# Kernel tuning notes

Hardware: AMD Instinct MI355X
Metric: run time of the kernel (lower is better)

Reference implementation:

```python
import jax, jax.numpy as jnp
import numpy as np

D_MODEL = 1024
NUM_HEADS = 16
D_K = D_MODEL // NUM_HEADS
THETA = 10000.0


def apply_rope(x, positions):
    # x: [b, h, s, d_k]; positions: [b, s] int32
    half = D_K // 2
    inv_freq = THETA ** (-jnp.arange(half, dtype=jnp.float32) * 2.0 / D_K)  # [half]
    angles = positions[:, None, :, None].astype(jnp.float32) * inv_freq  # [b,1,s,half]
    cos, sin = jnp.cos(angles), jnp.sin(angles)
    x1 = x[..., 0::2]  # even dims
    x2 = x[..., 1::2]  # odd dims
    out_even = x1 * cos - x2 * sin
    out_odd = x1 * sin + x2 * cos
    # re-interleave
    out = jnp.stack([out_even, out_odd], axis=-1)
    return out.reshape(x.shape)


def setup_inputs() -> dict:
    key = jax.random.key(0)
    ks = jax.random.split(key, 5)
    b, s = 2, 2048
    scale = 0.02
    return {
        "x": jax.random.normal(ks[0], (b, s, D_MODEL), dtype=jnp.float32),
        "Wq": jax.random.normal(ks[1], (D_MODEL, D_MODEL), dtype=jnp.float32) * scale,
        "Wk": jax.random.normal(ks[2], (D_MODEL, D_MODEL), dtype=jnp.float32) * scale,
        "Wv": jax.random.normal(ks[3], (D_MODEL, D_MODEL), dtype=jnp.float32) * scale,
        "Wo": jax.random.normal(ks[4], (D_MODEL, D_MODEL), dtype=jnp.float32) * scale,
    }


def reference(x, Wq, Wk, Wv, Wo):
    b, s, _ = x.shape
    # Linear(d, d) applied as x @ W^T (torch Linear convention, no bias)
    Q = x @ Wq.T
    K = x @ Wk.T
    V = x @ Wv.T
    # split heads: [b, s, h*d] -> [b, h, s, d]
    split = lambda t: t.reshape(b, s, NUM_HEADS, D_K).transpose(0, 2, 1, 3)
    Q, K, V = split(Q), split(K), split(V)
    positions = jnp.broadcast_to(jnp.arange(s, dtype=jnp.int32), (b, s))
    Q = apply_rope(Q, positions)
    K = apply_rope(K, positions)
    scores = jnp.einsum('bhqd,bhkd->bhqk', Q, K) / jnp.sqrt(jnp.float32(D_K))
    causal = jnp.tril(jnp.ones((s, s), dtype=bool))
    scores = jnp.where(causal[None, None], scores, -jnp.inf)
    attn = jax.nn.softmax(scores, axis=-1)
    out = jnp.einsum('bhqk,bhkd->bhqd', attn, V)
    out = out.transpose(0, 2, 1, 3).reshape(b, s, D_MODEL)
    return out @ Wo.T
```

## Files before the change

### kernel.cpp

```cpp
#include <hip/hip_runtime.h>

typedef __attribute__((ext_vector_type(8))) short bf16x8;
typedef __attribute__((ext_vector_type(4))) float f32x4;
typedef __attribute__((ext_vector_type(16))) float f32x16;

typedef const __attribute__((address_space(1))) unsigned int gu32;
typedef __attribute__((address_space(3))) unsigned int lu32;

__device__ __forceinline__ void async16(const void* g, void* l) {
  __builtin_amdgcn_global_load_lds((gu32*)g, (lu32*)l, 16, 0, 0);
}

__device__ __forceinline__ unsigned short f2bf(float f) {
  unsigned int u = __float_as_uint(f);
  u += 0x7fffu + ((u >> 16) & 1u);
  return (unsigned short)(u >> 16);
}
__device__ __forceinline__ float b2f(unsigned short s) {
  return __uint_as_float(((unsigned int)s) << 16);
}
__device__ __forceinline__ unsigned int cvtpk(float lo, float hi) {
  unsigned int w;
  asm("v_cvt_pk_bf16_f32 %0, %1, %2" : "=v"(w) : "v"(lo), "v"(hi));
  return w;
}
__device__ __forceinline__ void plswap(unsigned int& x, unsigned int& y) {
  asm("v_permlane32_swap_b32 %0, %1" : "+v"(x), "+v"(y));
}
__device__ __forceinline__ float max3f(float a, float b, float c) {
  float d;
  asm("v_max3_f32 %0, %1, %2, %3" : "=v"(d) : "v"(a), "v"(b), "v"(c));
  return d;
}

__global__ __launch_bounds__(256) void cvt_k(const float* __restrict__ in,
                                             unsigned short* __restrict__ out,
                                             int n4) {
  int i = blockIdx.x * 256 + threadIdx.x;
  if (i >= n4) return;
  float4 v = ((const float4*)in)[i];
  ushort4 o;
  o.x = f2bf(v.x); o.y = f2bf(v.y); o.z = f2bf(v.z); o.w = f2bf(v.w);
  ((ushort4*)out)[i] = o;
}

__global__ __launch_bounds__(256) void cvtw_k(const float* __restrict__ Wq,
                                              const float* __restrict__ Wk,
                                              const float* __restrict__ Wv,
                                              const float* __restrict__ Wo,
                                              unsigned short* __restrict__ Wb,
                                              unsigned short* __restrict__ Wob) {
  int i = blockIdx.x * 256 + threadIdx.x;
  int wsel = i >> 18;
  int j = i & 0x3FFFF;
  const float* src = (wsel == 0) ? Wq : (wsel == 1) ? Wk : (wsel == 2) ? Wv : Wo;
  unsigned short* dst = (wsel == 0) ? Wb : (wsel == 1) ? Wb + (1 << 20)
                       : (wsel == 2) ? Wb + (2 << 20) : Wob;
  float4 v = ((const float4*)src)[j];
  ushort4 o;
  o.x = f2bf(v.x); o.y = f2bf(v.y); o.z = f2bf(v.z); o.w = f2bf(v.w);
  ((ushort4*)dst)[j] = o;
}

template <int WRITE_F32>
__global__ __launch_bounds__(256) void gemm_bt(const unsigned short* __restrict__ A,
                                               const unsigned short* __restrict__ B,
                                               void* __restrict__ Cp, int N, int K) {
  __shared__ __align__(16) unsigned short Al[3][128 * 32];
  __shared__ __align__(16) unsigned short Bl[3][128 * 32];
  const int t = threadIdx.x;
  const int w = t >> 6, l = t & 63;
  const int wm = w >> 1, wn = w & 1;
  const int lr = l & 15, lg = l >> 4;
  const long bm = (long)blockIdx.x * 128, bn = (long)blockIdx.y * 128;
  const int srow = t >> 2;
  const int c8 = t & 3;
  const int KT = K >> 5;
  f32x4 acc[4][4] = {};

  auto STAGE = [&](int ts) {
    const int bi = ts % 3;
    const int k0 = ts * 32;
    #pragma unroll
    for (int r = 0; r < 2; ++r) {
      int row = r * 64 + srow;
      async16(&A[(bm + row) * (long)K + k0 + c8 * 8], &Al[bi][row * 32 + c8 * 8]);
      async16(&B[(bn + row) * (long)K + k0 + c8 * 8], &Bl[bi][row * 32 + c8 * 8]);
    }
  };

  STAGE(0);
  STAGE(1);
  for (int kt = 0; kt < KT; ++kt) {
    const int cur = kt % 3;
    if (kt < KT - 1) asm volatile("s_waitcnt vmcnt(4)" ::: "memory");
    else             asm volatile("s_waitcnt vmcnt(0)" ::: "memory");
    __builtin_amdgcn_s_barrier();
    __builtin_amdgcn_sched_barrier(0);
    if (kt + 2 < KT) STAGE(kt + 2);
    bf16x8 af[4], bf[4];
    #pragma unroll
    for (int i = 0; i < 4; ++i) {
      af[i] = *(const bf16x8*)&Al[cur][(wm * 64 + i * 16 + lr) * 32 + lg * 8];
      bf[i] = *(const bf16x8*)&Bl[cur][(wn * 64 + i * 16 + lr) * 32 + lg * 8];
    }
    #pragma unroll
    for (int i = 0; i < 4; ++i)
      #pragma unroll
      for (int j = 0; j < 4; ++j)
        acc[i][j] = __builtin_amdgcn_mfma_f32_16x16x32_bf16(af[i], bf[j], acc[i][j], 0, 0, 0);
  }
  #pragma unroll
  for (int i = 0; i < 4; ++i)
    #pragma unroll
    for (int j = 0; j < 4; ++j)
      #pragma unroll
      for (int r = 0; r < 4; ++r) {
        long row = bm + wm * 64 + i * 16 + lg * 4 + r;
        long col = bn + wn * 64 + j * 16 + lr;
        float v = acc[i][j][r];
        if (WRITE_F32) ((float*)Cp)[row * N + col] = v;
        else ((unsigned short*)Cp)[row * N + col] = f2bf(v);
      }
}

__global__ __launch_bounds__(256) void rope_k(unsigned short* __restrict__ QKV) {
  __shared__ float csl[32], snl[32];
  const int row = blockIdx.x;
  const int s = row & 2047;
  const int t = threadIdx.x;
  if (t < 32) {
    float invf = exp2f((float)t * (-13.287712379549449f / 32.0f));
    float sn, cs;
    sincosf((float)s * invf, &sn, &cs);
    csl[t] = cs; snl[t] = sn;
  }
  __syncthreads();
  const int col0 = (t < 128) ? t * 8 : 1024 + (t - 128) * 8;
  const int i0 = (t & 7) * 4;
  unsigned short* p = &QKV[(size_t)row * 3072 + col0];
  bf16x8 v = *(const bf16x8*)p;
  bf16x8 o;
  #pragma unroll
  for (int j = 0; j < 4; ++j) {
    float x1 = b2f((unsigned short)v[2 * j]);
    float x2 = b2f((unsigned short)v[2 * j + 1]);
    float cs = csl[i0 + j], sn = snl[i0 + j];
    o[2 * j]     = (short)f2bf(x1 * cs - x2 * sn);
    o[2 * j + 1] = (short)f2bf(x1 * sn + x2 * cs);
  }
  *(bf16x8*)p = o;
}

__global__ __launch_bounds__(256) void vtr_k(const unsigned short* __restrict__ QKV,
                                             unsigned short* __restrict__ Vt) {
  __shared__ unsigned short tl[64][66];
  const int kt = blockIdx.x;
  const int bh = blockIdx.y;
  const int b = bh >> 4, h = bh & 15;
  const int t = threadIdx.x;
  const int row = t >> 3, c8 = t & 7;
  #pragma unroll
  for (int r = 0; r < 2; ++r) {
    int k = r * 32 + row;
    bf16x8 v = *(const bf16x8*)&QKV[((long)b * 2048 + kt * 64 + k) * 3072 + 2048 + h * 64 + c8 * 8];
    #pragma unroll
    for (int j = 0; j < 8; ++j) tl[c8 * 8 + j][k] = (unsigned short)v[j];
  }
  __syncthreads();
  #pragma unroll
  for (int r = 0; r < 2; ++r) {
    int d = r * 32 + row;
    ushort4 a, bq;
    a.x = tl[d][c8 * 8 + 0]; a.y = tl[d][c8 * 8 + 1];
    a.z = tl[d][c8 * 8 + 2]; a.w = tl[d][c8 * 8 + 3];
    bq.x = tl[d][c8 * 8 + 4]; bq.y = tl[d][c8 * 8 + 5];
    bq.z = tl[d][c8 * 8 + 6]; bq.w = tl[d][c8 * 8 + 7];
    long off = ((long)bh * 64 + d) * 2048 + kt * 64 + c8 * 8;
    *(ushort4*)&Vt[off] = a;
    *(ushort4*)&Vt[off + 4] = bq;
  }
}

__global__ __launch_bounds__(256) void attn_k(const unsigned short* __restrict__ QKV,
                                              const unsigned short* __restrict__ VtG,
                                              unsigned short* __restrict__ O) {
  __shared__ __align__(16) unsigned short Kl[3][64 * 64];
  __shared__ __align__(16) unsigned short Vl[3][64 * 64];
  const int t = threadIdx.x;
  const int w = t >> 6, l = t & 63;
  const int q31 = l & 31, hi = l >> 5;
  const int bh = blockIdx.x;
  const int y = (int)blockIdx.y;
  const int qt = (y < 8) ? (15 - y) : (y - 8);
  const int b = bh >> 4, h = bh & 15;
  const int Qb = qt * 128;
  const long rowb = (long)b * 2048;
  const int L = 3072;
  const int NT = 2 * qt + 2;
  const float cexp = 0.125f * 1.4426950408889634f;

  const int qmy = Qb + 32 * w + q31;
  const long qgrow = rowb + qmy;
  const int ktmax = (Qb + 32 * w) >> 6;

  bf16x8 qf[4];
  #pragma unroll
  for (int dk = 0; dk < 4; ++dk)
    qf[dk] = *(const bf16x8*)&QKV[qgrow * L + h * 64 + dk * 16 + hi * 8];

  bf16x8 onesf;
  #pragma unroll
  for (int j = 0; j < 8; ++j) onesf[j] = (short)0x3F80;

  float m_ = -1e30f;
  f32x16 oa[2], la;
  #pragma unroll
  for (int r = 0; r < 16; ++r) { oa[0][r] = 0.0f; oa[1][r] = 0.0f; la[r] = 0.0f; }

  auto STAGE = [&](int ts) {
    const int bi = ts % 3;
    const long kb = rowb + (long)ts * 64;
    const long vrowb = (long)bh * 64;
    #pragma unroll
    for (int r = 0; r < 2; ++r) {
      int row = w * 16 + r * 8 + (l >> 3);
      int c8s = ((l & 7) ^ (row & 7)) * 8;
      async16(&QKV[(kb + row) * L + 1024 + h * 64 + c8s], &Kl[bi][row * 64 + (l & 7) * 8]);
      async16(&VtG[(vrowb + row) * 2048 + ts * 64 + c8s], &Vl[bi][row * 64 + (l & 7) * 8]);
    }
  };

  auto QK = [&](f32x16 (&st)[2], int bi) {
    #pragma unroll
    for (int kt2 = 0; kt2 < 2; ++kt2)
      #pragma unroll
      for (int r = 0; r < 16; ++r) st[kt2][r] = 0.0f;
    __builtin_amdgcn_s_setprio(1);
    #pragma unroll
    for (int dk = 0; dk < 4; ++dk)
      #pragma unroll
      for (int kt2 = 0; kt2 < 2; ++kt2) {
        int krow = kt2 * 32 + q31;
        bf16x8 kfr = *(const bf16x8*)&Kl[bi][krow * 64 + (((2 * dk + hi) ^ (krow & 7)) * 8)];
        st[kt2] = __builtin_amdgcn_mfma_f32_32x32x16_bf16(kfr, qf[dk], st[kt2], 0, 0, 0);
      }
    __builtin_amdgcn_s_setprio(0);
  };

  auto SMPV = [&](f32x16 (&st)[2], int kt) {
    if (kt == ktmax) {
      #pragma unroll
      for (int kt2 = 0; kt2 < 2; ++kt2)
        #pragma unroll
        for (int r = 0; r < 16; ++r) {
          int kg = kt * 64 + kt2 * 32 + (r & 3) + 8 * (r >> 2) + 4 * hi;
          if (kg > qmy) st[kt2][r] = -1e30f;
        }
    }
    float m0[8];
    #pragma unroll
    for (int i = 0; i < 8; ++i)
      m0[i] = max3f(st[0][i], st[0][i + 8], fmaxf(st[1][i], st[1][i + 8]));
    float mt = max3f(max3f(m0[0], m0[1], m0[2]), max3f(m0[3], m0[4], m0[5]),
                     fmaxf(m0[6], m0[7]));
    if (__any((mt - m_) * cexp > 8.0f)) {
      float mg = fmaxf(mt, __shfl_xor(mt, 32, 64));
      float mn = fmaxf(m_, mg);
      float al = __builtin_amdgcn_exp2f((m_ - mn) * cexp);
      m_ = mn;
      la[0] *= al;
      #pragma unroll
      for (int dt = 0; dt < 2; ++dt)
        #pragma unroll
        for (int r = 0; r < 16; ++r) oa[dt][r] *= al;
    }
    const float mc = m_ * cexp;
    #pragma unroll
    for (int kt2 = 0; kt2 < 2; ++kt2)
      #pragma unroll
      for (int r = 0; r < 16; ++r)
        st[kt2][r] = __builtin_amdgcn_exp2f(fmaf(st[kt2][r], cexp, -mc));
    bf16x8 pfr[4];
    #pragma unroll
    for (int ks = 0; ks < 4; ++ks) {
      int tt = ks >> 1, gX = 2 * (ks & 1), gY = gX + 1;
      unsigned int x1 = cvtpk(st[tt][4 * gX + 0], st[tt][4 * gX + 1]);
      unsigned int y1 = cvtpk(st[tt][4 * gY + 0], st[tt][4 * gY + 1]);
      plswap(x1, y1);
      unsigned int x2 = cvtpk(st[tt][4 * gX + 2], st[tt][4 * gX + 3]);
      unsigned int y2 = cvtpk(st[tt][4 * gY + 2], st[tt][4 * gY + 3]);
      plswap(x2, y2);
      union { unsigned int u[4]; bf16x8 b; } cc;
      cc.u[0] = x1; cc.u[1] = x2; cc.u[2] = y1; cc.u[3] = y2;
      pfr[ks] = cc.b;
    }
    const int vb = kt % 3;
    __builtin_amdgcn_s_setprio(1);
    #pragma unroll
    for (int ks = 0; ks < 4; ++ks) {
      la = __builtin_amdgcn_mfma_f32_32x32x16_bf16(onesf, pfr[ks], la, 0, 0, 0);
      #pragma unroll
      for (int dt = 0; dt < 2; ++dt) {
        int vrow = dt * 32 + q31;
        bf16x8 vf = *(const bf16x8*)&Vl[vb][vrow * 64 + (((2 * ks + hi) ^ (vrow & 7)) * 8)];
        oa[dt] = __builtin_amdgcn_mfma_f32_32x32x16_bf16(vf, pfr[ks], oa[dt], 0, 0, 0);
      }
    }
    __builtin_amdgcn_s_setprio(0);
  };

  f32x16 stA[2], stB[2];

  STAGE(0);
  STAGE(1);
  asm volatile("s_waitcnt vmcnt(4)" ::: "memory");
  __builtin_amdgcn_s_barrier();
  __builtin_amdgcn_sched_barrier(0);
  QK(stA, 0);

  auto STEP = [&](f32x16 (&cur)[2], f32x16 (&nxt)[2], int kt) {
    asm volatile("s_waitcnt vmcnt(0)" ::: "memory");
    __builtin_amdgcn_s_barrier();
    __builtin_amdgcn_sched_barrier(0);
    if (kt + 1 < NT && kt + 1 <= ktmax) QK(nxt, (kt + 1) % 3);
    if (kt + 2 < NT) STAGE(kt + 2);
    if (kt <= ktmax) SMPV(cur, kt);
  };

  int kt = 0;
  while (kt < NT) {
    STEP(stA, stB, kt); ++kt;
    if (kt < NT) { STEP(stB, stA, kt); ++kt; }
  }

  float inv = 1.0f / la[0];
  #pragma unroll
  for (int dt = 0; dt < 2; ++dt)
    #pragma unroll
    for (int g = 0; g < 4; ++g) {
      ushort4 o4;
      o4.x = f2bf(oa[dt][4 * g + 0] * inv);
      o4.y = f2bf(oa[dt][4 * g + 1] * inv);
      o4.z = f2bf(oa[dt][4 * g + 2] * inv);
      o4.w = f2bf(oa[dt][4 * g + 3] * inv);
      *(ushort4*)&O[qgrow * 1024 + h * 64 + dt * 32 + 8 * g + 4 * hi] = o4;
    }
}

extern "C" void kernel_launch(void* const* d_in, const int* in_sizes, int n_in,
                              void* d_out, int out_size, void* d_ws, size_t ws_size,
                              hipStream_t stream) {
  const float* x  = (const float*)d_in[0];
  const float* Wq = (const float*)d_in[1];
  const float* Wk = (const float*)d_in[2];
  const float* Wv = (const float*)d_in[3];
  const float* Wo = (const float*)d_in[4];
  char* ws = (char*)d_ws;
  unsigned short* xb   = (unsigned short*)(ws);
  unsigned short* Wb   = (unsigned short*)(ws + (8u << 20));
  unsigned short* Wob  = (unsigned short*)(ws + (14u << 20));
  unsigned short* QKVb = (unsigned short*)(ws + (16u << 20));
  unsigned short* Ob   = (unsigned short*)(ws + (40u << 20));
  unsigned short* Vtg  = xb;

  cvt_k<<<4096, 256, 0, stream>>>(x, xb, 4096 * 1024 / 4);
  cvtw_k<<<4096, 256, 0, stream>>>(Wq, Wk, Wv, Wo, Wb, Wob);

  gemm_bt<0><<<dim3(32, 24), 256, 0, stream>>>(xb, Wb, QKVb, 3072, 1024);
  rope_k<<<4096, 256, 0, stream>>>(QKVb);
  vtr_k<<<dim3(32, 32), 256, 0, stream>>>(QKVb, Vtg);
  attn_k<<<dim3(32, 16), 256, 0, stream>>>(QKVb, Vtg, Ob);
  gemm_bt<1><<<dim3(32, 8), 256, 0, stream>>>(Ob, Wob, d_out, 1024, 1024);
}
```

Measured before the change: 128.2 us.

## Merge conversion and rope/V-transpose launches; retile output projection GEMM

Folds the two fp32-to-bf16 conversion kernels into one launch and the RoPE and V-transpose kernels into one launch, with block index picking the role. The output projection moves to a new GEMM with 64x128 tiles and 128 threads, so it launches 512 blocks instead of 256 and fills more compute units. Fewer launches cut per-kernel gaps. In exchange, the smaller-tile GEMM reuses less data per block and the merged kernels carry branchy block roles.

New measurement: 123.3 us. 1.04x faster.

```diff
diff --git a/kernel.cpp b/kernel.cpp
--- a/kernel.cpp
+++ b/kernel.cpp
@@ -33,29 +33,28 @@
   return d;
 }
 
-__global__ __launch_bounds__(256) void cvt_k(const float* __restrict__ in,
-                                             unsigned short* __restrict__ out,
-                                             int n4) {
+__global__ __launch_bounds__(256) void cvt_all(const float* __restrict__ x,
+                                               const float* __restrict__ Wq,
+                                               const float* __restrict__ Wk,
+                                               const float* __restrict__ Wv,
+                                               const float* __restrict__ Wo,
+                                               unsigned short* __restrict__ xb,
+                                               unsigned short* __restrict__ Wb,
+                                               unsigned short* __restrict__ Wob) {
   int i = blockIdx.x * 256 + threadIdx.x;
-  if (i >= n4) return;
-  float4 v = ((const float4*)in)[i];
-  ushort4 o;
-  o.x = f2bf(v.x); o.y = f2bf(v.y); o.z = f2bf(v.z); o.w = f2bf(v.w);
-  ((ushort4*)out)[i] = o;
-}
-
-__global__ __launch_bounds__(256) void cvtw_k(const float* __restrict__ Wq,
-                                              const float* __restrict__ Wk,
-                                              const float* __restrict__ Wv,
-                                              const float* __restrict__ Wo,
-                                              unsigned short* __restrict__ Wb,
-                                              unsigned short* __restrict__ Wob) {
-  int i = blockIdx.x * 256 + threadIdx.x;
-  int wsel = i >> 18;
-  int j = i & 0x3FFFF;
-  const float* src = (wsel == 0) ? Wq : (wsel == 1) ? Wk : (wsel == 2) ? Wv : Wo;
-  unsigned short* dst = (wsel == 0) ? Wb : (wsel == 1) ? Wb + (1 << 20)
-                       : (wsel == 2) ? Wb + (2 << 20) : Wob;
+  const float* src;
+  unsigned short* dst;
+  int j;
+  if (i < (1 << 20)) {
+    src = x; dst = xb; j = i;
+  } else {
+    int k = i - (1 << 20);
+    int wsel = k >> 18;
+    j = k & 0x3FFFF;
+    src = (wsel == 0) ? Wq : (wsel == 1) ? Wk : (wsel == 2) ? Wv : Wo;
+    dst = (wsel == 0) ? Wb : (wsel == 1) ? Wb + (1 << 20)
+        : (wsel == 2) ? Wb + (2 << 20) : Wob;
+  }
   float4 v = ((const float4*)src)[j];
   ushort4 o;
   o.x = f2bf(v.x); o.y = f2bf(v.y); o.z = f2bf(v.z); o.w = f2bf(v.w);
@@ -124,61 +123,125 @@
       }
 }
 
-__global__ __launch_bounds__(256) void rope_k(unsigned short* __restrict__ QKV) {
-  __shared__ float csl[32], snl[32];
-  const int row = blockIdx.x;
-  const int s = row & 2047;
+__global__ __launch_bounds__(128) void gemm2_bt(const unsigned short* __restrict__ A,
+                                                const unsigned short* __restrict__ B,
+                                                float* __restrict__ Cp, int N, int K) {
+  __shared__ __align__(16) unsigned short Al[3][64 * 32];
+  __shared__ __align__(16) unsigned short Bl[3][128 * 32];
   const int t = threadIdx.x;
-  if (t < 32) {
-    float invf = exp2f((float)t * (-13.287712379549449f / 32.0f));
-    float sn, cs;
-    sincosf((float)s * invf, &sn, &cs);
-    csl[t] = cs; snl[t] = sn;
+  const int w = t >> 6, l = t & 63;
+  const int lr = l & 15, lg = l >> 4;
+  const long bm = (long)blockIdx.x * 64, bn = (long)blockIdx.y * 128;
+  const int KT = K >> 5;
+  f32x4 acc[4][4] = {};
+
+  auto STAGE = [&](int ts) {
+    const int bi = ts % 3;
+    const int k0 = ts * 32;
+    #pragma unroll
+    for (int r = 0; r < 2; ++r) {
+      int u = r * 128 + 64 * w + l;
+      int row = u >> 2, c8 = u & 3;
+      async16(&A[(bm + row) * (long)K + k0 + c8 * 8], &Al[bi][row * 32 + c8 * 8]);
+    }
+    #pragma unroll
+    for (int r = 0; r < 4; ++r) {
+      int u = r * 128 + 64 * w + l;
+      int row = u >> 2, c8 = u & 3;
+      async16(&B[(bn + row) * (long)K + k0 + c8 * 8], &Bl[bi][row * 32 + c8 * 8]);
+    }
+  };
+
+  STAGE(0);
+  STAGE(1);
+  for (int kt = 0; kt < KT; ++kt) {
+    const int cur = kt % 3;
+    if (kt < KT - 1) asm volatile("s_waitcnt vmcnt(6)" ::: "memory");
+    else             asm volatile("s_waitcnt vmcnt(0)" ::: "memory");
+    __builtin_amdgcn_s_barrier();
+    __builtin_amdgcn_sched_barrier(0);
+    if (kt + 2 < KT) STAGE(kt + 2);
+    bf16x8 af[4], bf[4];
+    #pragma unroll
+    for (int i = 0; i < 4; ++i) {
+      af[i] = *(const bf16x8*)&Al[cur][(i * 16 + lr) * 32 + lg * 8];
+      bf[i] = *(const bf16x8*)&Bl[cur][(w * 64 + i * 16 + lr) * 32 + lg * 8];
+    }
+    #pragma unroll
+    for (int i = 0; i < 4; ++i)
+      #pragma unroll
+      for (int j = 0; j < 4; ++j)
+        acc[i][j] = __builtin_amdgcn_mfma_f32_16x16x32_bf16(af[i], bf[j], acc[i][j], 0, 0, 0);
   }
-  __syncthreads();
-  const int col0 = (t < 128) ? t * 8 : 1024 + (t - 128) * 8;
-  const int i0 = (t & 7) * 4;
-  unsigned short* p = &QKV[(size_t)row * 3072 + col0];
-  bf16x8 v = *(const bf16x8*)p;
-  bf16x8 o;
-  #pragma unroll
-  for (int j = 0; j < 4; ++j) {
-    float x1 = b2f((unsigned short)v[2 * j]);
-    float x2 = b2f((unsigned short)v[2 * j + 1]);
-    float cs = csl[i0 + j], sn = snl[i0 + j];
-    o[2 * j]     = (short)f2bf(x1 * cs - x2 * sn);
-    o[2 * j + 1] = (short)f2bf(x1 * sn + x2 * cs);
-  }
-  *(bf16x8*)p = o;
-}
-
-__global__ __launch_bounds__(256) void vtr_k(const unsigned short* __restrict__ QKV,
-                                             unsigned short* __restrict__ Vt) {
+  #pragma unroll
+  for (int i = 0; i < 4; ++i)
+    #pragma unroll
+    for (int j = 0; j < 4; ++j)
+      #pragma unroll
+      for (int r = 0; r < 4; ++r) {
+        long row = bm + i * 16 + lg * 4 + r;
+        long col = bn + w * 64 + j * 16 + lr;
+        Cp[row * N + col] = acc[i][j][r];
+      }
+}
+
+__global__ __launch_bounds__(256) void ropevtr_k(unsigned short* __restrict__ QKV,
+                                                 unsigned short* __restrict__ Vt) {
   __shared__ unsigned short tl[64][66];
-  const int kt = blockIdx.x;
-  const int bh = blockIdx.y;
-  const int b = bh >> 4, h = bh & 15;
+  const int bx = blockIdx.x;
   const int t = threadIdx.x;
-  const int row = t >> 3, c8 = t & 7;
-  #pragma unroll
-  for (int r = 0; r < 2; ++r) {
-    int k = r * 32 + row;
-    bf16x8 v = *(const bf16x8*)&QKV[((long)b * 2048 + kt * 64 + k) * 3072 + 2048 + h * 64 + c8 * 8];
-    #pragma unroll
-    for (int j = 0; j < 8; ++j) tl[c8 * 8 + j][k] = (unsigned short)v[j];
-  }
-  __syncthreads();
-  #pragma unroll
-  for (int r = 0; r < 2; ++r) {
-    int d = r * 32 + row;
-    ushort4 a, bq;
-    a.x = tl[d][c8 * 8 + 0]; a.y = tl[d][c8 * 8 + 1];
-    a.z = tl[d][c8 * 8 + 2]; a.w = tl[d][c8 * 8 + 3];
-    bq.x = tl[d][c8 * 8 + 4]; bq.y = tl[d][c8 * 8 + 5];
-    bq.z = tl[d][c8 * 8 + 6]; bq.w = tl[d][c8 * 8 + 7];
-    long off = ((long)bh * 64 + d) * 2048 + kt * 64 + c8 * 8;
-    *(ushort4*)&Vt[off] = a;
-    *(ushort4*)&Vt[off + 4] = bq;
+  if (bx < 4096) {
+    float* csl = (float*)&tl[0][0];
+    float* snl = csl + 32;
+    const int row = bx;
+    const int s = row & 2047;
+    if (t < 32) {
+      float invf = exp2f((float)t * (-13.287712379549449f / 32.0f));
+      float sn, cs;
+      sincosf((float)s * invf, &sn, &cs);
+      csl[t] = cs; snl[t] = sn;
+    }
+    __syncthreads();
+    const int col0 = (t < 128) ? t * 8 : 1024 + (t - 128) * 8;
+    const int i0 = (t & 7) * 4;
+    unsigned short* p = &QKV[(size_t)row * 3072 + col0];
+    bf16x8 v = *(const bf16x8*)p;
+    bf16x8 o;
+    #pragma unroll
+    for (int j = 0; j < 4; ++j) {
+      float x1 = b2f((unsigned short)v[2 * j]);
+      float x2 = b2f((unsigned short)v[2 * j + 1]);
+      float cs = csl[i0 + j], sn = snl[i0 + j];
+      o[2 * j]     = (short)f2bf(x1 * cs - x2 * sn);
+      o[2 * j + 1] = (short)f2bf(x1 * sn + x2 * cs);
+    }
+    *(bf16x8*)p = o;
+  } else {
+    const int idx = bx - 4096;
+    const int kt = idx & 31;
+    const int bh = idx >> 5;
+    const int b = bh >> 4, h = bh & 15;
+    const int row = t >> 3, c8 = t & 7;
+    #pragma unroll
+    for (int r = 0; r < 2; ++r) {
+      int k = r * 32 + row;
+      bf16x8 v = *(const bf16x8*)&QKV[((long)b * 2048 + kt * 64 + k) * 3072 + 2048 + h * 64 + c8 * 8];
+      #pragma unroll
+      for (int j = 0; j < 8; ++j) tl[c8 * 8 + j][k] = (unsigned short)v[j];
+    }
+    __syncthreads();
+    #pragma unroll
+    for (int r = 0; r < 2; ++r) {
+      int d = r * 32 + row;
+      ushort4 a, bq;
+      a.x = tl[d][c8 * 8 + 0]; a.y = tl[d][c8 * 8 + 1];
+      a.z = tl[d][c8 * 8 + 2]; a.w = tl[d][c8 * 8 + 3];
+      bq.x = tl[d][c8 * 8 + 4]; bq.y = tl[d][c8 * 8 + 5];
+      bq.z = tl[d][c8 * 8 + 6]; bq.w = tl[d][c8 * 8 + 7];
+      long off = ((long)bh * 64 + d) * 2048 + kt * 64 + c8 * 8;
+      *(ushort4*)&Vt[off] = a;
+      *(ushort4*)&Vt[off + 4] = bq;
+    }
   }
 }
 
@@ -364,12 +427,9 @@
   unsigned short* Ob   = (unsigned short*)(ws + (40u << 20));
   unsigned short* Vtg  = xb;
 
-  cvt_k<<<4096, 256, 0, stream>>>(x, xb, 4096 * 1024 / 4);
-  cvtw_k<<<4096, 256, 0, stream>>>(Wq, Wk, Wv, Wo, Wb, Wob);
-
+  cvt_all<<<8192, 256, 0, stream>>>(x, Wq, Wk, Wv, Wo, xb, Wb, Wob);
   gemm_bt<0><<<dim3(32, 24), 256, 0, stream>>>(xb, Wb, QKVb, 3072, 1024);
-  rope_k<<<4096, 256, 0, stream>>>(QKVb);
-  vtr_k<<<dim3(32, 32), 256, 0, stream>>>(QKVb, Vtg);
+  ropevtr_k<<<5120, 256, 0, stream>>>(QKVb, Vtg);
   attn_k<<<dim3(32, 16), 256, 0, stream>>>(QKVb, Vtg, Ob);
-  gemm_bt<1><<<dim3(32, 8), 256, 0, stream>>>(Ob, Wob, d_out, 1024, 1024);
-}
+  gemm2_bt<<<dim3(64, 8), 128, 0, stream>>>(Ob, Wob, (float*)d_out, 1024, 1024);
+}
```
